# Kernel optimization log

Hardware: AMD Instinct MI355X
Metric: run time of the kernel (lower is better)

The kernel has to match this reference:

```python
import math
import jax, jax.numpy as jnp
import numpy as np

R, C, D, ORDER = 2048, 2048, 64, 3
O = ORDER + 1  # var_size


def setup_inputs() -> dict:
    key = jax.random.key(0)
    k1, k2, k3, k4, k5, k6 = jax.random.split(key, 6)
    return {
        "events": jax.random.randint(k1, (R, C), 0, 2, dtype=jnp.int32),
        "col_times": jax.random.uniform(k2, (C,), dtype=jnp.float32),
        "z_rows": jax.random.normal(k3, (O, R, D), dtype=jnp.float32),
        "z_cols": jax.random.normal(k4, (C, D), dtype=jnp.float32),
        "gamma_rows": jax.random.uniform(k5, (R,), dtype=jnp.float32),
        "gamma_cols": jax.random.uniform(k6, (C,), dtype=jnp.float32),
    }


def reference(events, col_times, z_rows, z_cols, gamma_rows, gamma_cols):
    o = z_rows.shape[0]
    facts = np.array([math.factorial(i) for i in range(o)], dtype=np.float32)
    # Taylor time-basis: coeffs[o, c] = t_c^o / o!   (replaces nested Python loops)
    coeffs = jnp.stack([col_times ** i for i in range(o)]) / facts[:, None]  # (O, C)
    # row positions at each column's time: (R, C, D)
    pos = jnp.einsum('ord,oc->rcd', z_rows, coeffs)
    diff = pos - z_cols[None, :, :]                        # (R, C, D)
    dist = jnp.sqrt(jnp.sum(diff * diff, axis=-1))         # (R, C) pairwise L2
    logit = gamma_rows[:, None] + gamma_cols[None, :] - dist
    # log p where p = 1 - E - (1-2E)*sigmoid(logit):
    #   E==1 -> log sigmoid(logit); E==0 -> log sigmoid(-logit)
    sign = jnp.where(events == 1, 1.0, -1.0).astype(logit.dtype)
    log_lik = jnp.sum(jax.nn.log_sigmoid(sign * logit))
    return -log_lik
```

## Files before the change

### kernel.cpp

```cpp
#include <hip/hip_runtime.h>
#include <hip/hip_bf16.h>
#include <math.h>

#define R_DIM 2048
#define C_DIM 2048
#define D_DIM 64
#define K_TOT 288

typedef __attribute__((ext_vector_type(8))) short short8;
typedef __attribute__((ext_vector_type(4))) float floatx4;

__device__ __forceinline__ ushort f2bf(float f) {
  unsigned u = __float_as_uint(f);
  return (ushort)((u + 0x7FFFu + ((u >> 16) & 1u)) >> 16);
}

__global__ void prep_kernel(const int* __restrict__ events,
                            const float* __restrict__ col_times,
                            const float* __restrict__ z_rows,
                            const float* __restrict__ z_cols,
                            ushort* __restrict__ Ab,
                            ushort* __restrict__ Bb,
                            float* __restrict__ nzc,
                            unsigned* __restrict__ Wb,
                            float* __restrict__ out) {
  const int b = blockIdx.x;
  const int t = threadIdx.x;
  const int lane = t & 63;

  if (b == 0 && t == 0) out[0] = 0.0f;

  const int4 e0 = *(const int4*)&events[(size_t)b * C_DIM + t * 4];
  const int4 e1 = *(const int4*)&events[(size_t)b * C_DIM + 1024 + t * 4];
  {
    unsigned w0 = ((unsigned)(e0.x & 1) | ((unsigned)(e0.y & 1) << 1) |
                   ((unsigned)(e0.z & 1) << 2) | ((unsigned)(e0.w & 1) << 3))
                  << ((t & 7) * 4);
    w0 |= __shfl_xor((int)w0, 1); w0 |= __shfl_xor((int)w0, 2);
    w0 |= __shfl_xor((int)w0, 4);
    if ((t & 7) == 0) Wb[b * 64 + (t >> 3)] = w0;
    unsigned w1 = ((unsigned)(e1.x & 1) | ((unsigned)(e1.y & 1) << 1) |
                   ((unsigned)(e1.z & 1) << 2) | ((unsigned)(e1.w & 1) << 3))
                  << ((t & 7) * 4);
    w1 |= __shfl_xor((int)w1, 1); w1 |= __shfl_xor((int)w1, 2);
    w1 |= __shfl_xor((int)w1, 4);
    if ((t & 7) == 0) Wb[b * 64 + 32 + (t >> 3)] = w1;
  }

  if (t < 64) {
    float zv[4];
#pragma unroll
    for (int o = 0; o < 4; ++o) {
      zv[o] = z_rows[(size_t)(o * R_DIM + b) * D_DIM + lane];
      Ab[(size_t)b * K_TOT + o * 64 + lane] = f2bf(zv[o]);
    }
    float g00 = zv[0] * zv[0], g01 = zv[0] * zv[1], g02 = zv[0] * zv[2],
          g03 = zv[0] * zv[3], g11 = zv[1] * zv[1], g12 = zv[1] * zv[2],
          g13 = zv[1] * zv[3], g22 = zv[2] * zv[2], g23 = zv[2] * zv[3],
          g33 = zv[3] * zv[3];
#pragma unroll
    for (int off = 32; off > 0; off >>= 1) {
      g00 += __shfl_xor(g00, off); g01 += __shfl_xor(g01, off);
      g02 += __shfl_xor(g02, off); g03 += __shfl_xor(g03, off);
      g11 += __shfl_xor(g11, off); g12 += __shfl_xor(g12, off);
      g13 += __shfl_xor(g13, off); g22 += __shfl_xor(g22, off);
      g23 += __shfl_xor(g23, off); g33 += __shfl_xor(g33, off);
    }
    if (lane == 0) {
      ushort* e = Ab + (size_t)b * K_TOT + 256;
      e[0] = f2bf(g00);  e[1] = f2bf(g01);  e[2] = f2bf(g02);  e[3] = f2bf(g03);
      e[4] = f2bf(g01);  e[5] = f2bf(g11);  e[6] = f2bf(g12);  e[7] = f2bf(g13);
      e[8] = f2bf(g02);  e[9] = f2bf(g12);  e[10] = f2bf(g22); e[11] = f2bf(g23);
      e[12] = f2bf(g03); e[13] = f2bf(g13); e[14] = f2bf(g23); e[15] = f2bf(g33);
    }
    if (lane < 16) Ab[(size_t)b * K_TOT + 272 + lane] = 0;
  } else if (t < 128) {
    const float tt = col_times[b];
    float cf[4];
    cf[0] = 1.0f; cf[1] = tt; cf[2] = tt * tt * 0.5f;
    cf[3] = cf[2] * tt * (1.0f / 3.0f);
    const float zc = z_cols[(size_t)b * D_DIM + lane];
#pragma unroll
    for (int o = 0; o < 4; ++o)
      Bb[(size_t)b * K_TOT + o * 64 + lane] = f2bf(-2.0f * cf[o] * zc);
    float q = zc * zc;
#pragma unroll
    for (int off = 32; off > 0; off >>= 1) q += __shfl_xor(q, off);
    if (lane == 0) {
      nzc[b] = q;
      ushort* e = Bb + (size_t)b * K_TOT + 256;
#pragma unroll
      for (int i = 0; i < 16; ++i) e[i] = f2bf(cf[i >> 2] * cf[i & 3]);
    }
    if (lane < 16) Bb[(size_t)b * K_TOT + 272 + lane] = 0;
  }
}

__launch_bounds__(256, 3)
__global__ void pair_kernel(const float* __restrict__ gamma_rows,
                            const float* __restrict__ gamma_cols,
                            const ushort* __restrict__ Ab,
                            const ushort* __restrict__ Bb,
                            const float* __restrict__ nzc,
                            const unsigned* __restrict__ Wb,
                            float* __restrict__ out) {
  __shared__ float red[4];
  const int t = threadIdx.x;
  const int widx = t >> 6, lane = t & 63;
  const int m0 = blockIdx.y * 64, c0 = blockIdx.x * 64;
  const int wm = widx & 1, wn = widx >> 1;
  const int lm = lane & 15, kg = lane >> 4;

  const ushort* a0p = Ab + (size_t)(m0 + wm * 32 + lm) * K_TOT + kg * 8;
  const ushort* a1p = a0p + 16 * K_TOT;
  const ushort* b0p = Bb + (size_t)(c0 + wn * 32 + lm) * K_TOT + kg * 8;
  const ushort* b1p = b0p + 16 * K_TOT;

  floatx4 acc[2][2];
#pragma unroll
  for (int i = 0; i < 2; ++i)
#pragma unroll
    for (int j = 0; j < 2; ++j) acc[i][j] = (floatx4){0.f, 0.f, 0.f, 0.f};

#pragma unroll
  for (int kt = 0; kt < 9; ++kt) {
    const short8 a0 = *(const short8*)(a0p + kt * 32);
    const short8 a1 = *(const short8*)(a1p + kt * 32);
    const short8 b0 = *(const short8*)(b0p + kt * 32);
    const short8 b1 = *(const short8*)(b1p + kt * 32);
    acc[0][0] = __builtin_amdgcn_mfma_f32_16x16x32_bf16(a0, b0, acc[0][0], 0, 0, 0);
    acc[0][1] = __builtin_amdgcn_mfma_f32_16x16x32_bf16(a0, b1, acc[0][1], 0, 0, 0);
    acc[1][0] = __builtin_amdgcn_mfma_f32_16x16x32_bf16(a1, b0, acc[1][0], 0, 0, 0);
    acc[1][1] = __builtin_amdgcn_mfma_f32_16x16x32_bf16(a1, b1, acc[1][1], 0, 0, 0);
  }

  float lsum = 0.0f;
#pragma unroll
  for (int nt = 0; nt < 2; ++nt) {
    const int c = c0 + wn * 32 + nt * 16 + lm;
    const float gc = gamma_cols[c];
    const float nz = nzc[c];
    const int cword = c >> 5, cbit = c & 31;
#pragma unroll
    for (int mt = 0; mt < 2; ++mt) {
      const int rbase = m0 + wm * 32 + mt * 16 + kg * 4;
#pragma unroll
      for (int j = 0; j < 4; ++j) {
        const int r = rbase + j;
        const float evf = (float)((Wb[r * 64 + cword] >> cbit) & 1u);
        const float d2 = acc[mt][nt][j] + nz;
        const float dist = sqrtf(fmaxf(d2, 0.0f));
        const float logit = gamma_rows[r] + gc - dist;
        lsum += fmaxf(logit, 0.0f) + __logf(1.0f + __expf(-fabsf(logit))) -
                evf * logit;
      }
    }
  }
#pragma unroll
  for (int off = 32; off > 0; off >>= 1) lsum += __shfl_down(lsum, off);
  if (lane == 0) red[widx] = lsum;
  __syncthreads();
  if (t == 0) atomicAdd(out, red[0] + red[1] + red[2] + red[3]);
}

extern "C" void kernel_launch(void* const* d_in, const int* in_sizes, int n_in,
                              void* d_out, int out_size, void* d_ws, size_t ws_size,
                              hipStream_t stream) {
  const int* events = (const int*)d_in[0];
  const float* col_times = (const float*)d_in[1];
  const float* z_rows = (const float*)d_in[2];
  const float* z_cols = (const float*)d_in[3];
  const float* gamma_rows = (const float*)d_in[4];
  const float* gamma_cols = (const float*)d_in[5];
  float* out = (float*)d_out;

  ushort* Ab = (ushort*)d_ws;
  ushort* Bb = Ab + (size_t)R_DIM * K_TOT;
  float* nzc = (float*)(Bb + (size_t)C_DIM * K_TOT);
  unsigned* Wb = (unsigned*)(nzc + C_DIM);

  prep_kernel<<<R_DIM, 256, 0, stream>>>(events, col_times, z_rows, z_cols, Ab,
                                         Bb, nzc, Wb, out);
  dim3 grid(C_DIM / 64, R_DIM / 64);
  pair_kernel<<<grid, 256, 0, stream>>>(gamma_rows, gamma_cols, Ab, Bb, nzc, Wb,
                                        out);
}
```

Measured before the change: 96.72 us.

## Fuse prep and pairwise kernels into one cooperative kernel with grid sync

Merges the preprocessing kernel and the pairwise MFMA kernel into a single cooperative launch of 512 blocks. Each block first packs events and builds the bf16 operands for 4 rows and columns, then does a grid-wide sync, then processes two 64x64 output tiles. This removes the second kernel launch and the gap between kernels. In exchange it adds a grid barrier, halves the number of pairwise blocks (each does two tiles serially), and lowers the occupancy target in launch bounds.

```diff
diff --git a/kernel.cpp b/kernel.cpp
--- a/kernel.cpp
+++ b/kernel.cpp
@@ -1,6 +1,9 @@
 #include <hip/hip_runtime.h>
 #include <hip/hip_bf16.h>
+#include <hip/hip_cooperative_groups.h>
 #include <math.h>
+
+namespace cg = cooperative_groups;
 
 #define R_DIM 2048
 #define C_DIM 2048
@@ -15,44 +18,53 @@
   return (ushort)((u + 0x7FFFu + ((u >> 16) & 1u)) >> 16);
 }
 
-__global__ void prep_kernel(const int* __restrict__ events,
-                            const float* __restrict__ col_times,
-                            const float* __restrict__ z_rows,
-                            const float* __restrict__ z_cols,
-                            ushort* __restrict__ Ab,
-                            ushort* __restrict__ Bb,
-                            float* __restrict__ nzc,
-                            unsigned* __restrict__ Wb,
-                            float* __restrict__ out) {
-  const int b = blockIdx.x;
+__launch_bounds__(256, 2)
+__global__ void fused_kernel(const int* __restrict__ events,
+                             const float* __restrict__ col_times,
+                             const float* __restrict__ z_rows,
+                             const float* __restrict__ z_cols,
+                             const float* __restrict__ gamma_rows,
+                             const float* __restrict__ gamma_cols,
+                             ushort* __restrict__ Ab,
+                             ushort* __restrict__ Bb,
+                             float* __restrict__ nzc,
+                             unsigned* __restrict__ Wb,
+                             float* __restrict__ out) {
+  __shared__ float red[4];
+  const int bid = blockIdx.x;
   const int t = threadIdx.x;
-  const int lane = t & 63;
+  const int widx = t >> 6, lane = t & 63;
 
-  if (b == 0 && t == 0) out[0] = 0.0f;
+  if (bid == 0 && t == 0) out[0] = 0.0f;
 
-  const int4 e0 = *(const int4*)&events[(size_t)b * C_DIM + t * 4];
-  const int4 e1 = *(const int4*)&events[(size_t)b * C_DIM + 1024 + t * 4];
-  {
+  const int r0 = bid * 4;
+
+#pragma unroll
+  for (int rr = 0; rr < 4; ++rr) {
+    const int r = r0 + rr;
+    const int4 e0 = *(const int4*)&events[(size_t)r * C_DIM + t * 4];
+    const int4 e1 = *(const int4*)&events[(size_t)r * C_DIM + 1024 + t * 4];
     unsigned w0 = ((unsigned)(e0.x & 1) | ((unsigned)(e0.y & 1) << 1) |
                    ((unsigned)(e0.z & 1) << 2) | ((unsigned)(e0.w & 1) << 3))
                   << ((t & 7) * 4);
     w0 |= __shfl_xor((int)w0, 1); w0 |= __shfl_xor((int)w0, 2);
     w0 |= __shfl_xor((int)w0, 4);
-    if ((t & 7) == 0) Wb[b * 64 + (t >> 3)] = w0;
+    if ((t & 7) == 0) Wb[r * 64 + (t >> 3)] = w0;
     unsigned w1 = ((unsigned)(e1.x & 1) | ((unsigned)(e1.y & 1) << 1) |
                    ((unsigned)(e1.z & 1) << 2) | ((unsigned)(e1.w & 1) << 3))
                   << ((t & 7) * 4);
     w1 |= __shfl_xor((int)w1, 1); w1 |= __shfl_xor((int)w1, 2);
     w1 |= __shfl_xor((int)w1, 4);
-    if ((t & 7) == 0) Wb[b * 64 + 32 + (t >> 3)] = w1;
+    if ((t & 7) == 0) Wb[r * 64 + 32 + (t >> 3)] = w1;
   }
 
-  if (t < 64) {
+  {
+    const int r = r0 + widx;
     float zv[4];
 #pragma unroll
     for (int o = 0; o < 4; ++o) {
-      zv[o] = z_rows[(size_t)(o * R_DIM + b) * D_DIM + lane];
-      Ab[(size_t)b * K_TOT + o * 64 + lane] = f2bf(zv[o]);
+      zv[o] = z_rows[(size_t)(o * R_DIM + r) * D_DIM + lane];
+      Ab[(size_t)r * K_TOT + o * 64 + lane] = f2bf(zv[o]);
     }
     float g00 = zv[0] * zv[0], g01 = zv[0] * zv[1], g02 = zv[0] * zv[2],
           g03 = zv[0] * zv[3], g11 = zv[1] * zv[1], g12 = zv[1] * zv[2],
@@ -67,95 +79,93 @@
       g23 += __shfl_xor(g23, off); g33 += __shfl_xor(g33, off);
     }
     if (lane == 0) {
-      ushort* e = Ab + (size_t)b * K_TOT + 256;
+      ushort* e = Ab + (size_t)r * K_TOT + 256;
       e[0] = f2bf(g00);  e[1] = f2bf(g01);  e[2] = f2bf(g02);  e[3] = f2bf(g03);
       e[4] = f2bf(g01);  e[5] = f2bf(g11);  e[6] = f2bf(g12);  e[7] = f2bf(g13);
       e[8] = f2bf(g02);  e[9] = f2bf(g12);  e[10] = f2bf(g22); e[11] = f2bf(g23);
       e[12] = f2bf(g03); e[13] = f2bf(g13); e[14] = f2bf(g23); e[15] = f2bf(g33);
     }
-    if (lane < 16) Ab[(size_t)b * K_TOT + 272 + lane] = 0;
-  } else if (t < 128) {
-    const float tt = col_times[b];
+    if (lane < 16) Ab[(size_t)r * K_TOT + 272 + lane] = 0;
+
+    const float tt = col_times[r];
     float cf[4];
     cf[0] = 1.0f; cf[1] = tt; cf[2] = tt * tt * 0.5f;
     cf[3] = cf[2] * tt * (1.0f / 3.0f);
-    const float zc = z_cols[(size_t)b * D_DIM + lane];
+    const float zc = z_cols[(size_t)r * D_DIM + lane];
 #pragma unroll
     for (int o = 0; o < 4; ++o)
-      Bb[(size_t)b * K_TOT + o * 64 + lane] = f2bf(-2.0f * cf[o] * zc);
+      Bb[(size_t)r * K_TOT + o * 64 + lane] = f2bf(-2.0f * cf[o] * zc);
     float q = zc * zc;
 #pragma unroll
     for (int off = 32; off > 0; off >>= 1) q += __shfl_xor(q, off);
     if (lane == 0) {
-      nzc[b] = q;
-      ushort* e = Bb + (size_t)b * K_TOT + 256;
+      nzc[r] = q;
+      ushort* e = Bb + (size_t)r * K_TOT + 256;
 #pragma unroll
       for (int i = 0; i < 16; ++i) e[i] = f2bf(cf[i >> 2] * cf[i & 3]);
     }
-    if (lane < 16) Bb[(size_t)b * K_TOT + 272 + lane] = 0;
+    if (lane < 16) Bb[(size_t)r * K_TOT + 272 + lane] = 0;
   }
-}
 
-__launch_bounds__(256, 3)
-__global__ void pair_kernel(const float* __restrict__ gamma_rows,
-                            const float* __restrict__ gamma_cols,
-                            const ushort* __restrict__ Ab,
-                            const ushort* __restrict__ Bb,
-                            const float* __restrict__ nzc,
-                            const unsigned* __restrict__ Wb,
-                            float* __restrict__ out) {
-  __shared__ float red[4];
-  const int t = threadIdx.x;
-  const int widx = t >> 6, lane = t & 63;
-  const int m0 = blockIdx.y * 64, c0 = blockIdx.x * 64;
+  __threadfence();
+  cg::this_grid().sync();
+  __threadfence();
+
   const int wm = widx & 1, wn = widx >> 1;
   const int lm = lane & 15, kg = lane >> 4;
-
-  const ushort* a0p = Ab + (size_t)(m0 + wm * 32 + lm) * K_TOT + kg * 8;
-  const ushort* a1p = a0p + 16 * K_TOT;
-  const ushort* b0p = Bb + (size_t)(c0 + wn * 32 + lm) * K_TOT + kg * 8;
-  const ushort* b1p = b0p + 16 * K_TOT;
-
-  floatx4 acc[2][2];
-#pragma unroll
-  for (int i = 0; i < 2; ++i)
-#pragma unroll
-    for (int j = 0; j < 2; ++j) acc[i][j] = (floatx4){0.f, 0.f, 0.f, 0.f};
+  float lsum = 0.0f;
 
 #pragma unroll
-  for (int kt = 0; kt < 9; ++kt) {
-    const short8 a0 = *(const short8*)(a0p + kt * 32);
-    const short8 a1 = *(const short8*)(a1p + kt * 32);
-    const short8 b0 = *(const short8*)(b0p + kt * 32);
-    const short8 b1 = *(const short8*)(b1p + kt * 32);
-    acc[0][0] = __builtin_amdgcn_mfma_f32_16x16x32_bf16(a0, b0, acc[0][0], 0, 0, 0);
-    acc[0][1] = __builtin_amdgcn_mfma_f32_16x16x32_bf16(a0, b1, acc[0][1], 0, 0, 0);
-    acc[1][0] = __builtin_amdgcn_mfma_f32_16x16x32_bf16(a1, b0, acc[1][0], 0, 0, 0);
-    acc[1][1] = __builtin_amdgcn_mfma_f32_16x16x32_bf16(a1, b1, acc[1][1], 0, 0, 0);
-  }
+  for (int ti = 0; ti < 2; ++ti) {
+    const int tile = bid + ti * 512;
+    const int m0 = (tile >> 5) * 64, c0 = (tile & 31) * 64;
 
-  float lsum = 0.0f;
+    const ushort* a0p = Ab + (size_t)(m0 + wm * 32 + lm) * K_TOT + kg * 8;
+    const ushort* a1p = a0p + 16 * K_TOT;
+    const ushort* b0p = Bb + (size_t)(c0 + wn * 32 + lm) * K_TOT + kg * 8;
+    const ushort* b1p = b0p + 16 * K_TOT;
+
+    floatx4 acc[2][2];
 #pragma unroll
-  for (int nt = 0; nt < 2; ++nt) {
-    const int c = c0 + wn * 32 + nt * 16 + lm;
-    const float gc = gamma_cols[c];
-    const float nz = nzc[c];
-    const int cword = c >> 5, cbit = c & 31;
+    for (int i = 0; i < 2; ++i)
 #pragma unroll
-    for (int mt = 0; mt < 2; ++mt) {
-      const int rbase = m0 + wm * 32 + mt * 16 + kg * 4;
+      for (int j = 0; j < 2; ++j) acc[i][j] = (floatx4){0.f, 0.f, 0.f, 0.f};
+
 #pragma unroll
-      for (int j = 0; j < 4; ++j) {
-        const int r = rbase + j;
-        const float evf = (float)((Wb[r * 64 + cword] >> cbit) & 1u);
-        const float d2 = acc[mt][nt][j] + nz;
-        const float dist = sqrtf(fmaxf(d2, 0.0f));
-        const float logit = gamma_rows[r] + gc - dist;
-        lsum += fmaxf(logit, 0.0f) + __logf(1.0f + __expf(-fabsf(logit))) -
-                evf * logit;
+    for (int kt = 0; kt < 9; ++kt) {
+      const short8 a0 = *(const short8*)(a0p + kt * 32);
+      const short8 a1 = *(const short8*)(a1p + kt * 32);
+      const short8 b0 = *(const short8*)(b0p + kt * 32);
+      const short8 b1 = *(const short8*)(b1p + kt * 32);
+      acc[0][0] = __builtin_amdgcn_mfma_f32_16x16x32_bf16(a0, b0, acc[0][0], 0, 0, 0);
+      acc[0][1] = __builtin_amdgcn_mfma_f32_16x16x32_bf16(a0, b1, acc[0][1], 0, 0, 0);
+      acc[1][0] = __builtin_amdgcn_mfma_f32_16x16x32_bf16(a1, b0, acc[1][0], 0, 0, 0);
+      acc[1][1] = __builtin_amdgcn_mfma_f32_16x16x32_bf16(a1, b1, acc[1][1], 0, 0, 0);
+    }
+
+#pragma unroll
+    for (int nt = 0; nt < 2; ++nt) {
+      const int c = c0 + wn * 32 + nt * 16 + lm;
+      const float gc = gamma_cols[c];
+      const float nz = nzc[c];
+      const int cword = c >> 5, cbit = c & 31;
+#pragma unroll
+      for (int mt = 0; mt < 2; ++mt) {
+        const int rbase = m0 + wm * 32 + mt * 16 + kg * 4;
+#pragma unroll
+        for (int j = 0; j < 4; ++j) {
+          const int r = rbase + j;
+          const float evf = (float)((Wb[r * 64 + cword] >> cbit) & 1u);
+          const float d2 = acc[mt][nt][j] + nz;
+          const float dist = sqrtf(fmaxf(d2, 0.0f));
+          const float logit = gamma_rows[r] + gc - dist;
+          lsum += fmaxf(logit, 0.0f) + __logf(1.0f + __expf(-fabsf(logit))) -
+                  evf * logit;
+        }
       }
     }
   }
+
 #pragma unroll
   for (int off = 32; off > 0; off >>= 1) lsum += __shfl_down(lsum, off);
   if (lane == 0) red[widx] = lsum;
@@ -179,9 +189,10 @@
   float* nzc = (float*)(Bb + (size_t)C_DIM * K_TOT);
   unsigned* Wb = (unsigned*)(nzc + C_DIM);
 
-  prep_kernel<<<R_DIM, 256, 0, stream>>>(events, col_times, z_rows, z_cols, Ab,
-                                         Bb, nzc, Wb, out);
-  dim3 grid(C_DIM / 64, R_DIM / 64);
-  pair_kernel<<<grid, 256, 0, stream>>>(gamma_rows, gamma_cols, Ab, Bb, nzc, Wb,
-                                        out);
+  void* args[] = {(void*)&events, (void*)&col_times, (void*)&z_rows,
+                  (void*)&z_cols, (void*)&gamma_rows, (void*)&gamma_cols,
+                  (void*)&Ab,     (void*)&Bb,         (void*)&nzc,
+                  (void*)&Wb,     (void*)&out};
+  hipLaunchCooperativeKernel((void*)fused_kernel, dim3(512), dim3(256), args, 0,
+                             stream);
 }
```

Result: slower. 209.2 us (+116.3%).
